# Optimization experiments

Measured on AMD Instinct MI355X. Metric: run time of the kernel, lower is better.

## Reference

```python
import math
import jax, jax.numpy as jnp
import numpy as np

B, S, H, N = 2, 2048, 2048, 16
HN = H // N
ALPHA = 32.0
MASK_VALUE = 10000.0


def setup_inputs() -> dict:
    key = jax.random.key(0)
    k1, k2, k3, k4, k5 = jax.random.split(key, 5)
    hidden_states = jax.random.normal(k1, (B, S, H), dtype=jnp.float32)
    # causal (left-to-right) multiplicative mask, broadcastable to [b, n, s, s]
    ltor_mask = jnp.tril(jnp.ones((S, S), dtype=jnp.float32))[None, None, :, :]
    # torch Linear params: y = x @ W.T + b
    w_qkv = jax.random.normal(k2, (3 * H, H), dtype=jnp.float32) * (1.0 / math.sqrt(H))
    b_qkv = jnp.zeros((3 * H,), dtype=jnp.float32)
    w_dense = jax.random.normal(k3, (H, H), dtype=jnp.float32) * (1.0 / math.sqrt(H))
    b_dense = jnp.zeros((H,), dtype=jnp.float32)
    return {"hidden_states": hidden_states, "ltor_mask": ltor_mask,
            "w_qkv": w_qkv, "b_qkv": b_qkv, "w_dense": w_dense, "b_dense": b_dense}


def reference(hidden_states, ltor_mask, w_qkv, b_qkv, w_dense, b_dense):
    b, s, h = hidden_states.shape
    # fused qkv projection
    qkv = hidden_states @ w_qkv.T + b_qkv                       # [b, s, 3h]
    q, k, v = jnp.split(qkv, 3, axis=-1)

    def heads(t):  # [b, s, h] -> [b, n, s, hn]
        return t.reshape(b, s, N, HN).transpose(0, 2, 1, 3)

    q, k, v = heads(q), heads(k), heads(v)
    # cogview pb_relax: scale query before matmul
    scores = jnp.einsum('bnsd,bntd->bnst', q / math.sqrt(HN), k)  # [b, n, s, s]
    m = ltor_mask[:, :, -s:]
    scores = scores * m - MASK_VALUE * (1.0 - m)
    # pb_relax max stabilization: per (batch, head) global max of scores/alpha
    scaled = scores / ALPHA
    maxes = jax.lax.stop_gradient(jnp.max(scaled, axis=(-2, -1), keepdims=True))
    scores = (scaled - maxes) * ALPHA
    probs = jax.nn.softmax(scores, axis=-1)
    ctx = jnp.einsum('bnst,bntd->bnsd', probs, v)                # [b, n, s, hn]
    ctx = ctx.transpose(0, 2, 1, 3).reshape(b, s, h)
    out = ctx @ w_dense.T + b_dense
    return out
```

## Files before the change

kernel.cpp:

```cpp
#include <hip/hip_runtime.h>

typedef __bf16 bf16_t;
typedef __bf16 bf16x8 __attribute__((ext_vector_type(8)));
typedef __bf16 bf16x4 __attribute__((ext_vector_type(4)));
typedef float f32x4 __attribute__((ext_vector_type(4)));

#define MFMA16(a, b, c) __builtin_amdgcn_mfma_f32_16x16x32_bf16((a), (b), (c), 0, 0, 0)

__device__ __forceinline__ void gload_lds16(const void* g, void* l) {
  __builtin_amdgcn_global_load_lds(
      (__attribute__((address_space(1))) void*)(g),
      (__attribute__((address_space(3))) void*)(l), 16, 0, 0);
}

__device__ __forceinline__ void block_bar() {
  asm volatile("" ::: "memory");
  __builtin_amdgcn_s_barrier();
  asm volatile("" ::: "memory");
}

__global__ __launch_bounds__(256) void cvt_f32_bf16(const float* __restrict__ in,
                                                    bf16_t* __restrict__ out, int n4) {
  int i = blockIdx.x * 256 + threadIdx.x;
  if (i >= n4) return;
  float4 v = ((const float4*)in)[i];
  bf16x4 o;
  o[0] = (bf16_t)v.x; o[1] = (bf16_t)v.y; o[2] = (bf16_t)v.z; o[3] = (bf16_t)v.w;
  ((bf16x4*)out)[i] = o;
}

template <int EPI>
__global__ __launch_bounds__(256) void gemm_bt(
    const bf16_t* __restrict__ A, const bf16_t* __restrict__ Bw,
    const float* __restrict__ bias,
    void* __restrict__ o0, void* __restrict__ o1, void* __restrict__ o2,
    int M, int N, int K) {
  __shared__ __attribute__((aligned(16))) bf16_t As[128][32];
  __shared__ __attribute__((aligned(16))) bf16_t Bs[128][32];
  const int tid = threadIdx.x;
  const int lane = tid & 63, wave = tid >> 6;
  const int wr = (wave >> 1) * 64, wc = (wave & 1) * 64;
  const int l15 = lane & 15, l4 = lane >> 4;
  const int bm = blockIdx.y * 128, bn = blockIdx.x * 128;

  f32x4 acc[4][4];
#pragma unroll
  for (int i = 0; i < 4; ++i)
#pragma unroll
    for (int j = 0; j < 4; ++j)
#pragma unroll
      for (int r = 0; r < 4; ++r) acc[i][j][r] = 0.0f;

  const int r0 = tid >> 2;
  const int co = (tid & 3) * 8;
  const bf16_t* gA = A + (size_t)(bm + r0) * K + co;
  const bf16_t* gB = Bw + (size_t)(bn + r0) * K + co;

  for (int kk = 0; kk < K; kk += 32) {
    gload_lds16(gA + kk, &As[r0][co]);
    gload_lds16(gA + kk + (size_t)64 * K, &As[r0 + 64][co]);
    gload_lds16(gB + kk, &Bs[r0][co]);
    gload_lds16(gB + kk + (size_t)64 * K, &Bs[r0 + 64][co]);
    asm volatile("s_waitcnt vmcnt(0)" ::: "memory");
    __syncthreads();
    bf16x8 a[4], b[4];
#pragma unroll
    for (int i = 0; i < 4; ++i) a[i] = *(const bf16x8*)(&As[wr + i * 16 + l15][l4 * 8]);
#pragma unroll
    for (int j = 0; j < 4; ++j) b[j] = *(const bf16x8*)(&Bs[wc + j * 16 + l15][l4 * 8]);
#pragma unroll
    for (int i = 0; i < 4; ++i)
#pragma unroll
      for (int j = 0; j < 4; ++j) acc[i][j] = MFMA16(a[i], b[j], acc[i][j]);
    __syncthreads();
  }

  if (EPI == 0) {
    bf16_t* qb = (bf16_t*)o0;
    bf16_t* kb = (bf16_t*)o1;
    bf16_t* vtb = (bf16_t*)o2;
    const int which = bn >> 11;
    const int head = (bn & 2047) >> 7;
#pragma unroll
    for (int i = 0; i < 4; ++i)
#pragma unroll
      for (int j = 0; j < 4; ++j)
#pragma unroll
        for (int r = 0; r < 4; ++r) {
          int m = bm + wr + i * 16 + l4 * 4 + r;
          int n = bn + wc + j * 16 + l15;
          float v = acc[i][j][r] + bias[n];
          int b = m >> 11, s = m & 2047;
          int d = n & 127;
          size_t hb = (size_t)(b * 16 + head);
          if (which == 0) {
            v *= 0.08838834764831845f;
            qb[(hb * 2048 + s) * 128 + d] = (bf16_t)v;
          } else if (which == 1) {
            kb[(hb * 2048 + s) * 128 + d] = (bf16_t)v;
          } else {
            vtb[(hb * 128 + d) * 2048 + s] = (bf16_t)v;
          }
        }
  } else {
    float* O = (float*)o0;
#pragma unroll
    for (int i = 0; i < 4; ++i)
#pragma unroll
      for (int j = 0; j < 4; ++j)
#pragma unroll
        for (int r = 0; r < 4; ++r) {
          int m = bm + wr + i * 16 + l4 * 4 + r;
          int n = bn + wc + j * 16 + l15;
          O[(size_t)m * N + n] = acc[i][j][r] + bias[n];
        }
  }
}

__global__ __launch_bounds__(512) void attn_kernel(
    const bf16_t* __restrict__ qbuf, const bf16_t* __restrict__ kbuf,
    const bf16_t* __restrict__ vtbuf, bf16_t* __restrict__ ctx) {
  __shared__ __attribute__((aligned(16))) bf16_t Ks[2][64][128];
  __shared__ __attribute__((aligned(16))) bf16_t Vts[2][128][64];
  __shared__ __attribute__((aligned(16))) bf16_t Ps[8][16][64];

  const int tid = threadIdx.x, lane = tid & 63, w = tid >> 6;
  const int l15 = lane & 15, l4 = lane >> 4;
  const int hb = blockIdx.y;
  const size_t hoff = (size_t)hb * 2048 * 128;
  const bf16_t* qh = qbuf + hoff;
  const bf16_t* kh = kbuf + hoff;
  const bf16_t* vh = vtbuf + hoff;
  const int b = hb >> 4, head = hb & 15;

  const int kr0 = tid >> 4, ks0 = tid & 15;
  const int vr0 = tid >> 3, vs0 = tid & 7;

  int buf = 0;

#pragma unroll 1
  for (int phase = 0; phase < 2; ++phase) {
    const int qt = phase == 0 ? blockIdx.x : 15 - blockIdx.x;
    const int q0 = qt * 128;
    const int nt = 2 * qt + 2;

    bf16x8 qa[4];
#pragma unroll
    for (int ks = 0; ks < 4; ++ks)
      qa[ks] = *(const bf16x8*)(qh + (size_t)(q0 + w * 16 + l15) * 128 + ks * 32 + l4 * 8);

    f32x4 accO[8];
#pragma unroll
    for (int df = 0; df < 8; ++df)
#pragma unroll
      for (int r = 0; r < 4; ++r) accO[df][r] = 0.0f;
    float mrow[4], lrow[4];
#pragma unroll
    for (int r = 0; r < 4; ++r) { mrow[r] = -1e30f; lrow[r] = 0.0f; }

    {
      const int kv0 = 0;
#pragma unroll
      for (int it = 0; it < 2; ++it) {
        int row = kr0 + it * 32, sch = ks0 ^ (row & 7);
        gload_lds16(kh + (size_t)(kv0 + row) * 128 + sch * 8, &Ks[buf][row][ks0 * 8]);
      }
#pragma unroll
      for (int it = 0; it < 2; ++it) {
        int row = vr0 + it * 64, sch = vs0 ^ (row & 7);
        gload_lds16(vh + (size_t)row * 2048 + kv0 + sch * 8, &Vts[buf][row][vs0 * 8]);
      }
    }

#pragma unroll 1
    for (int t = 0; t < nt; ++t) {
      const int kv0 = t * 64;
      if (t + 1 < nt) {
        const int kvn = (t + 1) * 64;
        const int nb = buf ^ 1;
#pragma unroll
        for (int it = 0; it < 2; ++it) {
          int row = kr0 + it * 32, sch = ks0 ^ (row & 7);
          gload_lds16(kh + (size_t)(kvn + row) * 128 + sch * 8, &Ks[nb][row][ks0 * 8]);
        }
#pragma unroll
        for (int it = 0; it < 2; ++it) {
          int row = vr0 + it * 64, sch = vs0 ^ (row & 7);
          gload_lds16(vh + (size_t)row * 2048 + kvn + sch * 8, &Vts[nb][row][vs0 * 8]);
        }
        asm volatile("s_waitcnt vmcnt(4)" ::: "memory");
      } else {
        asm volatile("s_waitcnt vmcnt(0)" ::: "memory");
      }
      block_bar();

      const bool active = (kv0 <= q0 + w * 16 + 15);
      if (active) {
        f32x4 sc[4];
#pragma unroll
        for (int nf = 0; nf < 4; ++nf) {
#pragma unroll
          for (int r = 0; r < 4; ++r) sc[nf][r] = 0.0f;
          int row = nf * 16 + l15;
#pragma unroll
          for (int ks = 0; ks < 4; ++ks) {
            int ch = (ks * 4 + l4) ^ (row & 7);
            bf16x8 kf = *(const bf16x8*)(&Ks[buf][row][ch * 8]);
            sc[nf] = MFMA16(qa[ks], kf, sc[nf]);
          }
        }

        if (kv0 + 63 > q0 + w * 16) {
#pragma unroll
          for (int nf = 0; nf < 4; ++nf)
#pragma unroll
            for (int r = 0; r < 4; ++r) {
              int qi = q0 + w * 16 + l4 * 4 + r;
              int kv = kv0 + nf * 16 + l15;
              if (kv > qi) sc[nf][r] = -1e30f;
            }
        }

        float tmax[4];
#pragma unroll
        for (int r = 0; r < 4; ++r)
          tmax[r] = fmaxf(fmaxf(sc[0][r], sc[1][r]), fmaxf(sc[2][r], sc[3][r]));
#pragma unroll
        for (int msk = 1; msk <= 8; msk <<= 1)
#pragma unroll
          for (int r = 0; r < 4; ++r)
            tmax[r] = fmaxf(tmax[r], __shfl_xor(tmax[r], msk, 64));

        bool defer = __all(tmax[0] <= mrow[0] + 8.0f && tmax[1] <= mrow[1] + 8.0f &&
                           tmax[2] <= mrow[2] + 8.0f && tmax[3] <= mrow[3] + 8.0f);
        if (!defer) {
          float scl[4];
#pragma unroll
          for (int r = 0; r < 4; ++r) {
            float mn = fmaxf(mrow[r], tmax[r]);
            scl[r] = __expf(mrow[r] - mn);
            mrow[r] = mn;
            lrow[r] *= scl[r];
          }
#pragma unroll
          for (int df = 0; df < 8; ++df)
#pragma unroll
            for (int r = 0; r < 4; ++r) accO[df][r] *= scl[r];
        }

        float rsum[4];
#pragma unroll
        for (int r = 0; r < 4; ++r) {
          float s0 = 0.0f;
#pragma unroll
          for (int nf = 0; nf < 4; ++nf) {
            float p = __expf(sc[nf][r] - mrow[r]);
            sc[nf][r] = p;
            s0 += p;
          }
          rsum[r] = s0;
        }
#pragma unroll
        for (int msk = 1; msk <= 8; msk <<= 1)
#pragma unroll
          for (int r = 0; r < 4; ++r) rsum[r] += __shfl_xor(rsum[r], msk, 64);
#pragma unroll
        for (int r = 0; r < 4; ++r) lrow[r] += rsum[r];

#pragma unroll
        for (int nf = 0; nf < 4; ++nf)
#pragma unroll
          for (int r = 0; r < 4; ++r) {
            int qi = l4 * 4 + r;
            int kv = nf * 16 + l15;
            int ch = (kv >> 3) ^ (qi & 7);
            Ps[w][qi][ch * 8 + (kv & 7)] = (bf16_t)sc[nf][r];
          }

        bf16x8 pa[2];
#pragma unroll
        for (int k2 = 0; k2 < 2; ++k2) {
          int ch = (k2 * 4 + l4) ^ (l15 & 7);
          pa[k2] = *(const bf16x8*)(&Ps[w][l15][ch * 8]);
        }
#pragma unroll
        for (int df = 0; df < 8; ++df) {
          int row = df * 16 + l15;
#pragma unroll
          for (int k2 = 0; k2 < 2; ++k2) {
            int ch = (k2 * 4 + l4) ^ (row & 7);
            bf16x8 vf = *(const bf16x8*)(&Vts[buf][row][ch * 8]);
            accO[df] = MFMA16(pa[k2], vf, accO[df]);
          }
        }
      }
      block_bar();
      buf ^= 1;
    }

    float inv[4];
#pragma unroll
    for (int r = 0; r < 4; ++r) inv[r] = 1.0f / lrow[r];
#pragma unroll
    for (int df = 0; df < 8; ++df)
#pragma unroll
      for (int r = 0; r < 4; ++r) {
        int s = q0 + w * 16 + l4 * 4 + r;
        int col = head * 128 + df * 16 + l15;
        ctx[((size_t)(b * 2048 + s)) * 2048 + col] = (bf16_t)(accO[df][r] * inv[r]);
      }
  }
}

extern "C" void kernel_launch(void* const* d_in, const int* in_sizes, int n_in,
                              void* d_out, int out_size, void* d_ws, size_t ws_size,
                              hipStream_t stream) {
  const float* hs = (const float*)d_in[0];
  const float* w_qkv = (const float*)d_in[2];
  const float* b_qkv = (const float*)d_in[3];
  const float* w_dense = (const float*)d_in[4];
  const float* b_dense = (const float*)d_in[5];
  float* out = (float*)d_out;

  const size_t SZ_HS = (size_t)4096 * 2048;
  const size_t SZ_WQKV = (size_t)6144 * 2048;
  const size_t SZ_WD = (size_t)2048 * 2048;
  const size_t SZ_H = (size_t)32 * 2048 * 128;

  char* ws = (char*)d_ws;
  bf16_t* A_ = (bf16_t*)ws;
  bf16_t* B_ = (bf16_t*)(ws + 2 * SZ_HS);
  bf16_t* Q_ = (bf16_t*)(ws + 2 * (SZ_HS + SZ_WQKV));
  bf16_t* K_ = Q_ + SZ_H;
  bf16_t* V_ = K_ + SZ_H;

  cvt_f32_bf16<<<(int)(SZ_HS / 4 / 256), 256, 0, stream>>>(hs, A_, (int)(SZ_HS / 4));
  cvt_f32_bf16<<<(int)(SZ_WQKV / 4 / 256), 256, 0, stream>>>(w_qkv, B_, (int)(SZ_WQKV / 4));

  gemm_bt<0><<<dim3(48, 32), 256, 0, stream>>>(A_, B_, b_qkv, Q_, K_, V_, 4096, 6144, 2048);

  cvt_f32_bf16<<<(int)(SZ_WD / 4 / 256), 256, 0, stream>>>(w_dense, A_, (int)(SZ_WD / 4));

  attn_kernel<<<dim3(8, 32), 512, 0, stream>>>(Q_, K_, V_, B_);

  gemm_bt<1><<<dim3(16, 32), 256, 0, stream>>>(B_, A_, b_dense, out, nullptr, nullptr,
                                               4096, 2048, 2048);
}
```

Baseline: 461.8 us.

## Double-buffer LDS tiles in GEMM to overlap global loads with MFMA

The GEMM kernel now keeps two LDS buffers for the A and B tiles. It issues the next K-tile's global-to-LDS loads before computing on the current tile, and waits with vmcnt(4) so only the older loads have to finish. This hides global memory latency behind the MFMA work. In exchange, LDS use doubles, which may reduce occupancy.

```diff
diff --git a/kernel.cpp b/kernel.cpp
--- a/kernel.cpp
+++ b/kernel.cpp
@@ -35,8 +35,8 @@
     const float* __restrict__ bias,
     void* __restrict__ o0, void* __restrict__ o1, void* __restrict__ o2,
     int M, int N, int K) {
-  __shared__ __attribute__((aligned(16))) bf16_t As[128][32];
-  __shared__ __attribute__((aligned(16))) bf16_t Bs[128][32];
+  __shared__ __attribute__((aligned(16))) bf16_t As[2][128][32];
+  __shared__ __attribute__((aligned(16))) bf16_t Bs[2][128][32];
   const int tid = threadIdx.x;
   const int lane = tid & 63, wave = tid >> 6;
   const int wr = (wave >> 1) * 64, wc = (wave & 1) * 64;
@@ -56,23 +56,38 @@
   const bf16_t* gA = A + (size_t)(bm + r0) * K + co;
   const bf16_t* gB = Bw + (size_t)(bn + r0) * K + co;
 
-  for (int kk = 0; kk < K; kk += 32) {
-    gload_lds16(gA + kk, &As[r0][co]);
-    gload_lds16(gA + kk + (size_t)64 * K, &As[r0 + 64][co]);
-    gload_lds16(gB + kk, &Bs[r0][co]);
-    gload_lds16(gB + kk + (size_t)64 * K, &Bs[r0 + 64][co]);
-    asm volatile("s_waitcnt vmcnt(0)" ::: "memory");
-    __syncthreads();
+  const int nt = K >> 5;
+
+  gload_lds16(gA, &As[0][r0][co]);
+  gload_lds16(gA + (size_t)64 * K, &As[0][r0 + 64][co]);
+  gload_lds16(gB, &Bs[0][r0][co]);
+  gload_lds16(gB + (size_t)64 * K, &Bs[0][r0 + 64][co]);
+
+#pragma unroll 1
+  for (int t = 0; t < nt; ++t) {
+    const int cb = t & 1;
+    if (t + 1 < nt) {
+      const int kk = (t + 1) << 5;
+      const int nb = cb ^ 1;
+      gload_lds16(gA + kk, &As[nb][r0][co]);
+      gload_lds16(gA + kk + (size_t)64 * K, &As[nb][r0 + 64][co]);
+      gload_lds16(gB + kk, &Bs[nb][r0][co]);
+      gload_lds16(gB + kk + (size_t)64 * K, &Bs[nb][r0 + 64][co]);
+      asm volatile("s_waitcnt vmcnt(4)" ::: "memory");
+    } else {
+      asm volatile("s_waitcnt vmcnt(0)" ::: "memory");
+    }
+    block_bar();
     bf16x8 a[4], b[4];
 #pragma unroll
-    for (int i = 0; i < 4; ++i) a[i] = *(const bf16x8*)(&As[wr + i * 16 + l15][l4 * 8]);
-#pragma unroll
-    for (int j = 0; j < 4; ++j) b[j] = *(const bf16x8*)(&Bs[wc + j * 16 + l15][l4 * 8]);
+    for (int i = 0; i < 4; ++i) a[i] = *(const bf16x8*)(&As[cb][wr + i * 16 + l15][l4 * 8]);
+#pragma unroll
+    for (int j = 0; j < 4; ++j) b[j] = *(const bf16x8*)(&Bs[cb][wc + j * 16 + l15][l4 * 8]);
 #pragma unroll
     for (int i = 0; i < 4; ++i)
 #pragma unroll
       for (int j = 0; j < 4; ++j) acc[i][j] = MFMA16(a[i], b[j], acc[i][j]);
-    __syncthreads();
+    block_bar();
   }
 
   if (EPI == 0) {
```

New measurement: 431.6 us. 1.07x faster.
